# Optimization experiments

Measured on AMD Instinct MI355X. Metric: run time of the kernel, lower is better.

The kernel has to match this reference:

```python
import jax, jax.numpy as jnp
import numpy as np

EMBED_DIM = 768
NUM_HEADS = 12
HEAD_DIM = EMBED_DIM // NUM_HEADS
B, T = 2, 2048


def setup_inputs() -> dict:
    key = jax.random.key(0)
    kx, kq, kqb, ko, kob = jax.random.split(key, 5)
    x = jax.random.normal(kx, (B, T, EMBED_DIM), dtype=jnp.float32)
    # xavier-uniform style params
    lim_qkv = float(np.sqrt(6.0 / (EMBED_DIM + 3 * EMBED_DIM)))
    qkv_kernel = jax.random.uniform(kq, (EMBED_DIM, 3 * EMBED_DIM), minval=-lim_qkv, maxval=lim_qkv, dtype=jnp.float32)
    qkv_bias = jnp.zeros((3 * EMBED_DIM,), dtype=jnp.float32)
    lim_o = float(np.sqrt(6.0 / (EMBED_DIM + EMBED_DIM)))
    o_kernel = jax.random.uniform(ko, (EMBED_DIM, EMBED_DIM), minval=-lim_o, maxval=lim_o, dtype=jnp.float32)
    o_bias = jnp.zeros((EMBED_DIM,), dtype=jnp.float32)
    return {"x": x, "qkv_kernel": qkv_kernel, "qkv_bias": qkv_bias, "o_kernel": o_kernel, "o_bias": o_bias}


def reference(x, qkv_kernel, qkv_bias, o_kernel, o_bias):
    b, t, d = x.shape
    # fused QKV projection
    qkv = jnp.einsum('btd,de->bte', x, qkv_kernel) + qkv_bias  # [B,T,3D]
    qkv = qkv.reshape(b, t, 3, NUM_HEADS, HEAD_DIM).transpose(2, 0, 3, 1, 4)  # [3,B,H,T,Dh]
    q, k, v = qkv[0], qkv[1], qkv[2]
    # naive attention: materializes full [B,H,T,T] scores (as in original)
    scale = 1.0 / np.sqrt(HEAD_DIM).astype(np.float32)
    attn_logits = jnp.einsum('bhqd,bhkd->bhqk', q, k) * scale
    attention = jax.nn.softmax(attn_logits, axis=-1)
    values = jnp.einsum('bhqk,bhkd->bhqd', attention, v)
    values = values.transpose(0, 2, 1, 3).reshape(b, t, d)  # [B,T,D]
    o = jnp.einsum('btd,de->bte', values, o_kernel) + o_bias
    return (o, attention)
```

## Files before the change

kernel.cpp:

```cpp
#include <hip/hip_runtime.h>
#include <hip/hip_bf16.h>
#include <hip/hip_fp16.h>

typedef _Float16 f16;
typedef _Float16 f16x4 __attribute__((ext_vector_type(4)));
typedef _Float16 f16x8 __attribute__((ext_vector_type(8)));
typedef float f32x4 __attribute__((ext_vector_type(4)));

#define MFMA16(a, b, c) __builtin_amdgcn_mfma_f32_16x16x32_f16(a, b, c, 0, 0, 0)

__device__ __forceinline__ float fexp2(float x) {
#if __has_builtin(__builtin_amdgcn_exp2f)
    return __builtin_amdgcn_exp2f(x);
#else
    return exp2f(x);
#endif
}

typedef __attribute__((address_space(1))) const void gconst_t;
typedef __attribute__((address_space(3))) void lds_t;
__device__ __forceinline__ void gload16(const f16* g, f16* l) {
    __builtin_amdgcn_global_load_lds((gconst_t*)g, (lds_t*)l, 16, 0, 0);
}

__device__ __forceinline__ void transpose_body(const float* __restrict__ in, f16* __restrict__ out,
                                               int K, int N, int n0, int k0, int t,
                                               f16 (*tile)[72]) {
    int r = t >> 2, cb = (t & 3) * 16;
    const float* src = in + (size_t)(k0 + r) * N + n0 + cb;
#pragma unroll
    for (int j = 0; j < 4; ++j) {
        float4 v = ((const float4*)src)[j];
        tile[r][cb + 4 * j + 0] = (f16)v.x;
        tile[r][cb + 4 * j + 1] = (f16)v.y;
        tile[r][cb + 4 * j + 2] = (f16)v.z;
        tile[r][cb + 4 * j + 3] = (f16)v.w;
    }
    __syncthreads();
    int nl = t >> 2, kb = (t & 3) * 16;
    f16* dst = out + (size_t)(n0 + nl) * K + k0 + kb;
#pragma unroll
    for (int j = 0; j < 2; ++j) {
        f16x8 o;
#pragma unroll
        for (int e = 0; e < 8; ++e) o[e] = tile[kb + 8 * j + e][nl];
        *(f16x8*)(dst + 8 * j) = o;
    }
}

__global__ __launch_bounds__(256) void k_prep(const float* __restrict__ x,
                                              const float* __restrict__ wqkv,
                                              const float* __restrict__ wo,
                                              f16* __restrict__ xh, f16* __restrict__ wqkv_t,
                                              f16* __restrict__ wo_t) {
    __shared__ f16 tile[64][72];
    int bid = blockIdx.x, t = threadIdx.x;
    if (bid < 3072) {
        int i = bid * 256 + t;
        float4 v = ((const float4*)x)[i];
        f16x4 o = {(f16)v.x, (f16)v.y, (f16)v.z, (f16)v.w};
        ((f16x4*)xh)[i] = o;
    } else if (bid < 3504) {
        int idx = bid - 3072;
        transpose_body(wqkv, wqkv_t, 768, 2304, (idx % 36) * 64, (idx / 36) * 64, t, tile);
    } else {
        int idx = bid - 3504;
        transpose_body(wo, wo_t, 768, 768, (idx % 12) * 64, (idx / 12) * 64, t, tile);
    }
}

__device__ __forceinline__ void gemm_core(const f16* __restrict__ A, const f16* __restrict__ Bt,
                                          int m0, int n0, int lane, int w, int wr, int wc,
                                          f16* As, f16* Bs, f32x4 acc[4][4]) {
    int prow = lane >> 2, pc = lane & 3;
    int lrow = prow ^ ((prow >> 2) & 1);
    int lcol = (pc ^ (lrow & 3)) * 8;
    int rsw = (lane & 7) << 3;
    for (int kt = 0; kt < 24; ++kt) {
        const f16* ab = A + (size_t)(m0 + w * 32 + lrow) * 768 + kt * 32 + lcol;
        const f16* bb = Bt + (size_t)(n0 + w * 32 + lrow) * 768 + kt * 32 + lcol;
        gload16(ab, As + (w * 32) * 32);
        gload16(ab + (size_t)16 * 768, As + (w * 32 + 16) * 32);
        gload16(bb, Bs + (w * 32) * 32);
        gload16(bb + (size_t)16 * 768, Bs + (w * 32 + 16) * 32);
        __syncthreads();
        f16x8 a[4], b[4];
#pragma unroll
        for (int i = 0; i < 4; ++i) {
            int idx = (wr * 64 + i * 16 + (lane & 15)) * 32 + (lane >> 4) * 8;
            a[i] = *(const f16x8*)(As + (idx ^ rsw));
        }
#pragma unroll
        for (int j = 0; j < 4; ++j) {
            int idx = (wc * 64 + j * 16 + (lane & 15)) * 32 + (lane >> 4) * 8;
            b[j] = *(const f16x8*)(Bs + (idx ^ rsw));
        }
#pragma unroll
        for (int i = 0; i < 4; ++i)
#pragma unroll
            for (int j = 0; j < 4; ++j) acc[i][j] = MFMA16(a[i], b[j], acc[i][j]);
        __syncthreads();
    }
}

__global__ __launch_bounds__(256) void k_qkv_gemm(const f16* __restrict__ A, const f16* __restrict__ Bt,
                                                  const float* __restrict__ bias,
                                                  f16* __restrict__ Qh, f16* __restrict__ Kf,
                                                  f16* __restrict__ Vf) {
    __shared__ __align__(16) f16 As[128 * 32];
    __shared__ __align__(16) f16 Bs[128 * 32];
    int m0 = blockIdx.x * 128, n0 = blockIdx.y * 128;
    int t = threadIdx.x, lane = t & 63, w = t >> 6;
    int wr = w >> 1, wc = w & 1;
    f32x4 zero = {0.f, 0.f, 0.f, 0.f};
    f32x4 acc[4][4];
#pragma unroll
    for (int i = 0; i < 4; ++i)
#pragma unroll
        for (int j = 0; j < 4; ++j) acc[i][j] = zero;

    gemm_core(A, Bt, m0, n0, lane, w, wr, wc, As, Bs, acc);

    const float QSCALE = 0.18033688011112042f;
#pragma unroll
    for (int j = 0; j < 4; ++j) {
        int n = n0 + wc * 64 + j * 16 + (lane & 15);
        int which = n / 768;
        int rem = n - which * 768;
        int h = rem >> 6, d = rem & 63;
        float bv = bias[n];
#pragma unroll
        for (int i = 0; i < 4; ++i) {
            int m = m0 + wr * 64 + i * 16 + ((lane >> 4) << 2);
            int bb = m >> 11, tt = m & 2047;
            int bh = bb * 12 + h;
            if (which == 2) {
                int kt = tt >> 6;
                int half = (tt & 63) >> 5, hi = (tt & 31) >> 3, e0 = tt & 7;
                int jd = d >> 4, lo = d & 15;
                size_t addr = (((size_t)bh * 32 + kt) * 8 + jd * 2 + half) * 512 +
                              (size_t)(hi * 16 + lo) * 8 + e0;
                f16x4 pk;
#pragma unroll
                for (int r = 0; r < 4; ++r) pk[r] = (f16)(acc[i][j][r] + bv);
                *(f16x4*)(Vf + addr) = pk;
            } else if (which == 0) {
#pragma unroll
                for (int r = 0; r < 4; ++r)
                    Qh[((size_t)bh * 2048 + tt + r) * 64 + d] = (f16)((acc[i][j][r] + bv) * QSCALE);
            } else {
                int half = d >> 5, hi = (d & 31) >> 3, e = d & 7;
#pragma unroll
                for (int r = 0; r < 4; ++r) {
                    int tr = tt + r;
                    int kt = tr >> 6, row = tr & 63;
                    int s = row >> 4, lo = row & 15;
                    size_t addr = (((size_t)bh * 32 + kt) * 8 + s * 2 + half) * 512 +
                                  (size_t)(hi * 16 + lo) * 8 + e;
                    Kf[addr] = (f16)(acc[i][j][r] + bv);
                }
            }
        }
    }
}

__global__ __launch_bounds__(256) void k_o_gemm(const f16* __restrict__ A, const f16* __restrict__ Bt,
                                                const float* __restrict__ bias,
                                                float* __restrict__ out) {
    __shared__ __align__(16) f16 As[128 * 32];
    __shared__ __align__(16) f16 Bs[128 * 32];
    int m0 = blockIdx.x * 128, n0 = blockIdx.y * 128;
    int t = threadIdx.x, lane = t & 63, w = t >> 6;
    int wr = w >> 1, wc = w & 1;
    f32x4 zero = {0.f, 0.f, 0.f, 0.f};
    f32x4 acc[4][4];
#pragma unroll
    for (int i = 0; i < 4; ++i)
#pragma unroll
        for (int j = 0; j < 4; ++j) acc[i][j] = zero;

    gemm_core(A, Bt, m0, n0, lane, w, wr, wc, As, Bs, acc);

#pragma unroll
    for (int j = 0; j < 4; ++j) {
        int n = n0 + wc * 64 + j * 16 + (lane & 15);
        float bv = bias[n];
#pragma unroll
        for (int i = 0; i < 4; ++i) {
            int m = m0 + wr * 64 + i * 16 + ((lane >> 4) << 2);
#pragma unroll
            for (int r = 0; r < 4; ++r) out[(size_t)(m + r) * 768 + n] = acc[i][j][r] + bv;
        }
    }
}

__global__ __launch_bounds__(256) void k_lsum(const f16* __restrict__ Qh, const f16* __restrict__ Kf,
                                              float* __restrict__ lpart) {
    int qt = blockIdx.x, bh = blockIdx.y, kc = blockIdx.z;
    int q0 = qt * 64;
    int t = threadIdx.x, lane = t & 63, w = t >> 6;
    const f16* qbase = Qh + ((size_t)bh * 2048 + q0 + w * 16) * 64;
    const f16* kfb = Kf + (size_t)bh * 32 * 4096 + (size_t)lane * 8;

    f16x8 aq[2];
#pragma unroll
    for (int f = 0; f < 2; ++f)
        aq[f] = *(const f16x8*)(qbase + (size_t)(lane & 15) * 64 + f * 32 + (lane >> 4) * 8);
    f32x4 zero = {0.f, 0.f, 0.f, 0.f};

    auto LOADK = [&](f16x8* dst, int kt) {
        const f16* kp = kfb + (size_t)kt * 4096;
#pragma unroll
        for (int f = 0; f < 8; ++f) dst[f] = *(const f16x8*)(kp + f * 512);
    };
    auto QKTS = [&](const f16x8* kf, f32x4* s4) {
        __builtin_amdgcn_s_setprio(1);
#pragma unroll
        for (int s = 0; s < 4; ++s) {
            s4[s] = MFMA16(kf[2 * s], aq[0], zero);
            s4[s] = MFMA16(kf[2 * s + 1], aq[1], s4[s]);
        }
        __builtin_amdgcn_s_setprio(0);
    };

    f16x8 ka[8], kb2[8];
    float lsum = 0.f;
    int base = kc * 8;
    LOADK(ka, base);
    for (int i = 0; i < 8; i += 2) {
        f32x4 s4[4];
        LOADK(kb2, base + i + 1);
        QKTS(ka, s4);
#pragma unroll
        for (int s = 0; s < 4; ++s)
#pragma unroll
            for (int r = 0; r < 4; ++r) lsum += fexp2(s4[s][r]);
        LOADK(ka, base + ((i + 2) & 7));
        QKTS(kb2, s4);
#pragma unroll
        for (int s = 0; s < 4; ++s)
#pragma unroll
            for (int r = 0; r < 4; ++r) lsum += fexp2(s4[s][r]);
    }
    lsum += __shfl_xor(lsum, 16, 64);
    lsum += __shfl_xor(lsum, 32, 64);
    float* lp = lpart + (size_t)kc * 49152 + (size_t)bh * 2048 + q0 + w * 16;
    if (lane < 16) lp[lane] = lsum;
}

__global__ __launch_bounds__(256, 3) void k_attn(const f16* __restrict__ Qh, const f16* __restrict__ Kf,
                                                 const f16* __restrict__ Vf,
                                                 const float* __restrict__ lpart,
                                                 float* __restrict__ attn, f16* __restrict__ valh) {
    __shared__ __align__(16) f16 KV[2][8192];
    __shared__ __align__(16) float Ps32_all[4][16 * 68];
    int orig = blockIdx.x;
    int swz = (orig & 7) * 96 + (orig >> 3);
    int bh = swz >> 5, qt = swz & 31;
    int q0 = qt * 64;
    int t = threadIdx.x, lane = t & 63, w = t >> 6;

    const f16* qbase = Qh + ((size_t)bh * 2048 + q0 + w * 16) * 64;
    const f16* kfT = Kf + (size_t)bh * 32 * 4096;
    const f16* vfT = Vf + (size_t)bh * 32 * 4096;

    f16x8 aq[2];
#pragma unroll
    for (int f = 0; f < 2; ++f)
        aq[f] = *(const f16x8*)(qbase + (size_t)(lane & 15) * 64 + f * 32 + (lane >> 4) * 8);
    f32x4 zero = {0.f, 0.f, 0.f, 0.f};

    float linv;
    {
        size_t qoff = (size_t)bh * 2048 + q0 + w * 16 + (lane & 15);
        float s = 0.f;
#pragma unroll
        for (int kc = 0; kc < 4; ++kc) s += lpart[(size_t)kc * 49152 + qoff];
        linv = 1.0f / s;
    }

    auto STAGE = [&](int buf, int kt) {
        const f16* kp = kfT + (size_t)kt * 4096 + (size_t)lane * 8;
        const f16* vp = vfT + (size_t)kt * 4096 + (size_t)lane * 8;
        f16* kb = &KV[buf][0];
        f16* vb = &KV[buf][4096];
        gload16(kp + (2 * w) * 512, kb + (2 * w) * 512);
        gload16(kp + (2 * w + 1) * 512, kb + (2 * w + 1) * 512);
        gload16(vp + (2 * w) * 512, vb + (2 * w) * 512);
        gload16(vp + (2 * w + 1) * 512, vb + (2 * w + 1) * 512);
    };

    f32x4 accv[4];
#pragma unroll
    for (int j = 0; j < 4; ++j) accv[j] = zero;
    float* Ps = Ps32_all[w];
    float* attn_base = attn + ((size_t)bh * 2048 + q0 + w * 16) * 2048;

    STAGE(0, 0);
    __syncthreads();
    int cur = 0;
    for (int kt = 0; kt < 32; ++kt) {
        if (kt < 31) STAGE(cur ^ 1, kt + 1);
        const f16* Ks = &KV[cur][0];
        const f16* Vs = &KV[cur][4096];
        f32x4 s4[4];
        __builtin_amdgcn_s_setprio(1);
#pragma unroll
        for (int s = 0; s < 4; ++s) {
            f16x8 k0 = *(const f16x8*)(Ks + (2 * s) * 512 + lane * 8);
            f16x8 k1 = *(const f16x8*)(Ks + (2 * s + 1) * 512 + lane * 8);
            s4[s] = MFMA16(k0, aq[0], zero);
            s4[s] = MFMA16(k1, aq[1], s4[s]);
        }
        __builtin_amdgcn_s_setprio(0);
#pragma unroll
        for (int s = 0; s < 4; ++s) {
            f32x4 pv;
#pragma unroll
            for (int r = 0; r < 4; ++r) pv[r] = fexp2(s4[s][r]) * linv;
            *(f32x4*)(Ps + (lane & 15) * 68 + s * 16 + (lane >> 4) * 4) = pv;
        }
        f16x8 pa[2];
#pragma unroll
        for (int hh = 0; hh < 2; ++hh) {
            const float* pr = Ps + (lane & 15) * 68 + hh * 32 + (lane >> 4) * 8;
            f32x4 lo = *(const f32x4*)(pr);
            f32x4 hi = *(const f32x4*)(pr + 4);
            f16x8 pf = {(f16)lo[0], (f16)lo[1], (f16)lo[2], (f16)lo[3],
                        (f16)hi[0], (f16)hi[1], (f16)hi[2], (f16)hi[3]};
            pa[hh] = pf;
        }
        float* ab = attn_base + kt * 64;
#pragma unroll
        for (int i = 0; i < 4; ++i) {
            int row = i * 4 + (lane >> 4);
            int col = (lane & 15) * 4;
            f32x4 v = *(const f32x4*)(Ps + row * 68 + col);
            *(f32x4*)(ab + (size_t)row * 2048 + col) = v;
        }
        __builtin_amdgcn_s_setprio(1);
#pragma unroll
        for (int jd = 0; jd < 4; ++jd) {
            f16x8 v0 = *(const f16x8*)(Vs + (2 * jd) * 512 + lane * 8);
            f16x8 v1 = *(const f16x8*)(Vs + (2 * jd + 1) * 512 + lane * 8);
            accv[jd] = MFMA16(pa[0], v0, accv[jd]);
            accv[jd] = MFMA16(pa[1], v1, accv[jd]);
        }
        __builtin_amdgcn_s_setprio(0);
        __syncthreads();
        cur ^= 1;
    }

    int b = bh / 12, h = bh - b * 12;
#pragma unroll
    for (int j = 0; j < 4; ++j) {
#pragma unroll
        for (int r = 0; r < 4; ++r) {
            int rowg = b * 2048 + q0 + w * 16 + (lane >> 4) * 4 + r;
            int col = h * 64 + j * 16 + (lane & 15);
            valh[(size_t)rowg * 768 + col] = (f16)accv[j][r];
        }
    }
}

extern "C" void kernel_launch(void* const* d_in, const int* in_sizes, int n_in,
                              void* d_out, int out_size, void* d_ws, size_t ws_size,
                              hipStream_t stream) {
    const float* x = (const float*)d_in[0];
    const float* wqkv = (const float*)d_in[1];
    const float* bqkv = (const float*)d_in[2];
    const float* wo = (const float*)d_in[3];
    const float* bo = (const float*)d_in[4];

    float* out_o = (float*)d_out;
    float* out_attn = out_o + (size_t)2 * 2048 * 768;

    f16* ws = (f16*)d_ws;
    f16* xh = ws;
    f16* wqkv_t = xh + 3145728;
    f16* wo_t = wqkv_t + 1769472;
    f16* Qh = wo_t + 589824;
    f16* Kf = Qh + 3145728;
    f16* Vf = Kf + 3145728;
    f16* valh = Vf + 3145728;
    float* lpart = (float*)(valh + 3145728);

    k_prep<<<3648, 256, 0, stream>>>(x, wqkv, wo, xh, wqkv_t, wo_t);
    k_qkv_gemm<<<dim3(32, 18), 256, 0, stream>>>(xh, wqkv_t, bqkv, Qh, Kf, Vf);
    k_lsum<<<dim3(32, 24, 4), 256, 0, stream>>>(Qh, Kf, lpart);
    k_attn<<<768, 256, 0, stream>>>(Qh, Kf, Vf, lpart, out_attn, valh);
    k_o_gemm<<<dim3(32, 6), 256, 0, stream>>>(valh, wo_t, bo, out_o);
}
```

Before: 188.4 us.

## Stage K through LDS in lsum kernel and defer attention-row stores

The row-sum kernel now stages K tiles into a double-buffered LDS buffer with async global-to-LDS loads instead of loading them straight into registers, which cuts register pressure but adds a block barrier per tile. The attention kernel keeps each tile's probability rows in registers and writes them to global memory one iteration later, so the large fp32 attention-matrix stores overlap the next tile's MFMA work. This costs 16 extra VGPRs held across iterations, which could lower occupancy.

New measurement: 184.4 us, median of 2. 2.1% less time.

```diff
diff --git a/kernel.cpp b/kernel.cpp
--- a/kernel.cpp
+++ b/kernel.cpp
@@ -196,11 +196,12 @@
 
 __global__ __launch_bounds__(256) void k_lsum(const f16* __restrict__ Qh, const f16* __restrict__ Kf,
                                               float* __restrict__ lpart) {
+    __shared__ __align__(16) f16 KR[2][4096];
     int qt = blockIdx.x, bh = blockIdx.y, kc = blockIdx.z;
     int q0 = qt * 64;
     int t = threadIdx.x, lane = t & 63, w = t >> 6;
     const f16* qbase = Qh + ((size_t)bh * 2048 + q0 + w * 16) * 64;
-    const f16* kfb = Kf + (size_t)bh * 32 * 4096 + (size_t)lane * 8;
+    const f16* kfT = Kf + (size_t)bh * 32 * 4096;
 
     f16x8 aq[2];
 #pragma unroll
@@ -208,40 +209,38 @@
         aq[f] = *(const f16x8*)(qbase + (size_t)(lane & 15) * 64 + f * 32 + (lane >> 4) * 8);
     f32x4 zero = {0.f, 0.f, 0.f, 0.f};
 
-    auto LOADK = [&](f16x8* dst, int kt) {
-        const f16* kp = kfb + (size_t)kt * 4096;
-#pragma unroll
-        for (int f = 0; f < 8; ++f) dst[f] = *(const f16x8*)(kp + f * 512);
-    };
-    auto QKTS = [&](const f16x8* kf, f32x4* s4) {
+    int base = kc * 8;
+    auto STAGEK = [&](f16* buf, int kt) {
+        const f16* kp = kfT + (size_t)kt * 4096 + (size_t)lane * 8;
+        gload16(kp + (2 * w) * 512, buf + (2 * w) * 512);
+        gload16(kp + (2 * w + 1) * 512, buf + (2 * w + 1) * 512);
+    };
+    float lsum = 0.f;
+    auto COMP = [&](const f16* Ks) {
+        f32x4 s4[4];
         __builtin_amdgcn_s_setprio(1);
 #pragma unroll
         for (int s = 0; s < 4; ++s) {
-            s4[s] = MFMA16(kf[2 * s], aq[0], zero);
-            s4[s] = MFMA16(kf[2 * s + 1], aq[1], s4[s]);
+            f16x8 k0 = *(const f16x8*)(Ks + (2 * s) * 512 + lane * 8);
+            f16x8 k1 = *(const f16x8*)(Ks + (2 * s + 1) * 512 + lane * 8);
+            s4[s] = MFMA16(k0, aq[0], zero);
+            s4[s] = MFMA16(k1, aq[1], s4[s]);
         }
         __builtin_amdgcn_s_setprio(0);
-    };
-
-    f16x8 ka[8], kb2[8];
-    float lsum = 0.f;
-    int base = kc * 8;
-    LOADK(ka, base);
-    for (int i = 0; i < 8; i += 2) {
-        f32x4 s4[4];
-        LOADK(kb2, base + i + 1);
-        QKTS(ka, s4);
 #pragma unroll
         for (int s = 0; s < 4; ++s)
 #pragma unroll
             for (int r = 0; r < 4; ++r) lsum += fexp2(s4[s][r]);
-        LOADK(ka, base + ((i + 2) & 7));
-        QKTS(kb2, s4);
-#pragma unroll
-        for (int s = 0; s < 4; ++s)
-#pragma unroll
-            for (int r = 0; r < 4; ++r) lsum += fexp2(s4[s][r]);
-    }
+    };
+
+    STAGEK(KR[0], base);
+    __syncthreads();
+    for (int i = 0; i < 8; ++i) {
+        if (i < 7) STAGEK(KR[(i + 1) & 1], base + i + 1);
+        COMP(KR[i & 1]);
+        __syncthreads();
+    }
+
     lsum += __shfl_xor(lsum, 16, 64);
     lsum += __shfl_xor(lsum, 32, 64);
     float* lp = lpart + (size_t)kc * 49152 + (size_t)bh * 2048 + q0 + w * 16;
@@ -279,15 +278,13 @@
         linv = 1.0f / s;
     }
 
-    auto STAGE = [&](int buf, int kt) {
+    auto STAGE = [&](f16* kb, int kt) {
         const f16* kp = kfT + (size_t)kt * 4096 + (size_t)lane * 8;
         const f16* vp = vfT + (size_t)kt * 4096 + (size_t)lane * 8;
-        f16* kb = &KV[buf][0];
-        f16* vb = &KV[buf][4096];
         gload16(kp + (2 * w) * 512, kb + (2 * w) * 512);
         gload16(kp + (2 * w + 1) * 512, kb + (2 * w + 1) * 512);
-        gload16(vp + (2 * w) * 512, vb + (2 * w) * 512);
-        gload16(vp + (2 * w + 1) * 512, vb + (2 * w + 1) * 512);
+        gload16(vp + (2 * w) * 512, kb + 4096 + (2 * w) * 512);
+        gload16(vp + (2 * w + 1) * 512, kb + 4096 + (2 * w + 1) * 512);
     };
 
     f32x4 accv[4];
@@ -295,14 +292,18 @@
     for (int j = 0; j < 4; ++j) accv[j] = zero;
     float* Ps = Ps32_all[w];
     float* attn_base = attn + ((size_t)bh * 2048 + q0 + w * 16) * 2048;
-
-    STAGE(0, 0);
-    __syncthreads();
-    int cur = 0;
-    for (int kt = 0; kt < 32; ++kt) {
-        if (kt < 31) STAGE(cur ^ 1, kt + 1);
-        const f16* Ks = &KV[cur][0];
-        const f16* Vs = &KV[cur][4096];
+    f32x4 srow[4];
+
+    auto EMIT = [&](int kt) {
+        float* ab = attn_base + kt * 64;
+#pragma unroll
+        for (int i = 0; i < 4; ++i)
+            *(f32x4*)(ab + (size_t)(i * 4 + (lane >> 4)) * 2048 + (lane & 15) * 4) = srow[i];
+    };
+
+    auto COMPUTE = [&](const f16* buf, int kt) {
+        const f16* Ks = buf;
+        const f16* Vs = buf + 4096;
         f32x4 s4[4];
         __builtin_amdgcn_s_setprio(1);
 #pragma unroll
@@ -330,14 +331,9 @@
                         (f16)hi[0], (f16)hi[1], (f16)hi[2], (f16)hi[3]};
             pa[hh] = pf;
         }
-        float* ab = attn_base + kt * 64;
-#pragma unroll
-        for (int i = 0; i < 4; ++i) {
-            int row = i * 4 + (lane >> 4);
-            int col = (lane & 15) * 4;
-            f32x4 v = *(const f32x4*)(Ps + row * 68 + col);
-            *(f32x4*)(ab + (size_t)row * 2048 + col) = v;
-        }
+#pragma unroll
+        for (int i = 0; i < 4; ++i)
+            srow[i] = *(const f32x4*)(Ps + (i * 4 + (lane >> 4)) * 68 + (lane & 15) * 4);
         __builtin_amdgcn_s_setprio(1);
 #pragma unroll
         for (int jd = 0; jd < 4; ++jd) {
@@ -347,9 +343,19 @@
             accv[jd] = MFMA16(pa[1], v1, accv[jd]);
         }
         __builtin_amdgcn_s_setprio(0);
+    };
+
+    STAGE(KV[0], 0);
+    __syncthreads();
+    int cur = 0;
+    for (int kt = 0; kt < 32; ++kt) {
+        if (kt < 31) STAGE(KV[cur ^ 1], kt + 1);
+        if (kt > 0) EMIT(kt - 1);
+        COMPUTE(KV[cur], kt);
         __syncthreads();
         cur ^= 1;
     }
+    EMIT(31);
 
     int b = bh / 12, h = bh - b * 12;
 #pragma unroll
```
